# Kernel tuning notes

Measured on AMD Instinct MI355X. Metric: run time of the kernel, lower is better.

Reference implementation:

```python
import jax, jax.numpy as jnp
import numpy as np

ARITY = 4
DEPTH = 8  # leaves live at level DEPTH; levels 0..DEPTH, BFS layout
N_NODES = (ARITY ** (DEPTH + 1) - 1) // (ARITY - 1)  # 87381
V, E, H = 1024, 128, 128


def _offset(level):
    return (ARITY ** level - 1) // (ARITY - 1)


def _lstm_final(seq, w_ih, w_hh, b):
    # seq: [T, B, E_in] -> final hidden state [B, H] (torch LSTM cell, gate order i,f,g,o)
    B = seq.shape[1]
    Hh = w_hh.shape[1]
    xg = jnp.einsum('tbe,ge->tbg', seq, w_ih) + b  # precompute input projections [T,B,4H]

    def step(carry, g_t):
        h, c = carry
        g = g_t + h @ w_hh.T
        i, f, gg, o = jnp.split(g, 4, axis=-1)
        c = jax.nn.sigmoid(f) * c + jax.nn.sigmoid(i) * jnp.tanh(gg)
        h = jax.nn.sigmoid(o) * jnp.tanh(c)
        return (h, c), None

    init = (jnp.zeros((B, Hh), seq.dtype), jnp.zeros((B, Hh), seq.dtype))
    (h, _), _ = jax.lax.scan(step, init, xg)
    return h


def setup_inputs():
    key = jax.random.key(0)
    ks = jax.random.split(key, 12)
    s = 0.1
    labels = jax.random.randint(ks[0], (N_NODES,), 0, V)
    emb = jax.random.normal(ks[1], (V, E), jnp.float32) * s
    emb = emb.at[0].set(0.0)  # padding_idx=0
    mk = lambda k, shp: jax.random.normal(k, shp, jnp.float32) * s
    return {
        'labels': labels, 'emb': emb,
        'w_ih_f': mk(ks[2], (4 * H, E)), 'w_hh_f': mk(ks[3], (4 * H, H)),
        'b_ih_f': mk(ks[4], (4 * H,)), 'b_hh_f': mk(ks[5], (4 * H,)),
        'w_ih_b': mk(ks[6], (4 * H, E)), 'w_hh_b': mk(ks[7], (4 * H, H)),
        'b_ih_b': mk(ks[8], (4 * H,)), 'b_hh_b': mk(ks[9], (4 * H,)),
        'lin_w': mk(ks[10], (E, 2 * H)), 'lin_b': mk(ks[11], (E,)),
    }


def reference(labels, emb, w_ih_f, w_hh_f, b_ih_f, b_hh_f,
              w_ih_b, w_hh_b, b_ih_b, b_hh_b, lin_w, lin_b):
    # padding row is frozen at zero (padding_idx=0 semantics)
    emb = emb.at[0].set(0.0)
    node_emb = emb[labels]  # [N, E]
    bf = b_ih_f + b_hh_f
    bb = b_ih_b + b_hh_b
    enc = jnp.zeros((N_NODES, E), node_emb.dtype)
    # level-by-level dynamic batching: identical math to per-node recursion
    for level in range(DEPTH, -1, -1):
        start = _offset(level)
        count = ARITY ** level
        x = node_emb[start:start + count]  # [C, E]
        if level == DEPTH:
            seq = jnp.stack([x, x])  # leaves: [node, node] -> [2, C, E]
        else:
            cstart = _offset(level + 1)
            ch = enc[cstart:cstart + count * ARITY]
            ch = ch.reshape(count, ARITY, E).transpose(1, 0, 2)  # [K, C, E]
            seq = jnp.concatenate([x[None], ch, x[None]], axis=0)  # [K+2, C, E]
        h_f = _lstm_final(seq, w_ih_f, w_hh_f, bf)          # forward direction
        h_b = _lstm_final(seq[::-1], w_ih_b, w_hh_b, bb)    # reverse direction
        out = jnp.tanh(jnp.concatenate([h_f, h_b], axis=-1) @ lin_w.T + lin_b)
        enc = enc.at[start:start + count].set(out)
    return enc[0]  # root encoding, shape [E]
```

## Files before the change

### kernel.cpp

```cpp
#include <hip/hip_runtime.h>
#include <hip/hip_bf16.h>

typedef __attribute__((ext_vector_type(8))) short bf16x8;
typedef __attribute__((ext_vector_type(4))) float f32x4;

__device__ __forceinline__ ushort f2bf(float f) {
  union { float f; unsigned u; } v; v.f = f;
  unsigned u = v.u;
  return (ushort)((u + 0x7FFFu + ((u >> 16) & 1u)) >> 16);
}
__device__ __forceinline__ float bf2f(ushort u) {
  union { unsigned u; float f; } v; v.u = ((unsigned)u) << 16;
  return v.f;
}
__device__ __forceinline__ float fsig(float x) {
  return __builtin_amdgcn_rcpf(1.0f + __expf(-x));
}
__device__ __forceinline__ float ftnh(float x) {
  float e = __expf(2.0f * x);
  return 1.0f - 2.0f * __builtin_amdgcn_rcpf(e + 1.0f);
}
__device__ __forceinline__ f32x4 MF(bf16x8 a, bf16x8 b, f32x4 c) {
  return __builtin_amdgcn_mfma_f32_16x16x32_bf16(a, b, c, 0, 0, 0);
}

__global__ __launch_bounds__(256) void repack_all2(
    const float* __restrict__ wihf, const float* __restrict__ whhf,
    const float* __restrict__ wihb, const float* __restrict__ whhb,
    const float* __restrict__ emb, const float* __restrict__ linw,
    ushort* __restrict__ wall) {
  int i = blockIdx.x * 256 + threadIdx.x;
  if (i < 131072) {
    int e = i & 7, f = (i >> 3) & 15, lane = (i >> 7) & 63, w = (i >> 13) & 7,
        d = (i >> 16) & 1;
    int nt = f >> 2, kk = f & 3;
    int pcol = w * 64 + nt * 16 + (lane & 15);
    int g = (pcol >> 4) & 3, h = (pcol >> 6) * 16 + (pcol & 15);
    int k = kk * 32 + (lane >> 4) * 8 + e;
    const float* src = d ? whhb : whhf;
    wall[i] = f2bf(src[(g * 128 + h) * 128 + k]);
  } else if (i < 262144) {
    int r = i - 131072;
    int e = r & 7, lane = (r >> 3) & 63, kk = (r >> 9) & 3, j = (r >> 11) & 7,
        wq = (r >> 14) & 3, d = (r >> 16) & 1;
    int pcol = wq * 128 + j * 16 + (lane & 15);
    int g = (pcol >> 4) & 3, h = (pcol >> 6) * 16 + (pcol & 15);
    int k = kk * 32 + (lane >> 4) * 8 + e;
    const float* src = d ? wihb : wihf;
    wall[i] = f2bf(src[(g * 128 + h) * 128 + k]);
  } else if (i < 294912) {
    int r = i - 262144;
    int e = r & 7, lane = (r >> 3) & 63, kk = (r >> 9) & 7, w = (r >> 12) & 7;
    int col = w * 16 + (lane & 15);
    int k = kk * 32 + (lane >> 4) * 8 + e;
    wall[i] = f2bf(linw[col * 256 + k]);
  } else if (i < 425984) {
    int r = i - 294912;
    wall[i] = f2bf(emb[r]);
  }
}

__global__ __launch_bounds__(512) void vocab_all(
    const ushort* __restrict__ emb_bf, const ushort* __restrict__ wihrep,
    const ushort* __restrict__ whhrep, const ushort* __restrict__ linrep,
    const float* __restrict__ linb, const float* __restrict__ bihf,
    const float* __restrict__ bhhf, const float* __restrict__ bihb,
    const float* __restrict__ bhhb, ushort* __restrict__ gxv,
    ushort* __restrict__ gcv) {
  __shared__ __align__(16) ushort sT[2048];
  __shared__ __align__(16) ushort sGx[16384];
  __shared__ __align__(16) ushort sHf[2][2048];
  __shared__ __align__(16) ushort sH[2048];
  const int tid = threadIdx.x;
  const int w = tid >> 6, l = tid & 63, hlo = l & 15, lg = l >> 4;
  const int r0 = lg * 4, k0 = lg * 8;
  const int hcol = w * 16 + hlo;
  const int v0 = blockIdx.x * 16;

  {
    int row = tid >> 5, col0 = (tid & 31) * 4;
    *(ushort4*)(sT + row * 128 + (col0 ^ ((row & 7) << 3))) =
        *(const ushort4*)(emb_bf + (size_t)(v0 + row) * 128 + col0);
  }
  __syncthreads();
  const int dd = w >> 2, wq = w & 3;
  {
    const ushort* wp = wihrep + (size_t)(dd * 4 + wq) * 16384 + l * 8;
    bf16x8 wfv[32];
#pragma unroll
    for (int j = 0; j < 8; ++j)
#pragma unroll
      for (int kk = 0; kk < 4; ++kk)
        wfv[j * 4 + kk] = *(const bf16x8*)(wp + j * 2048 + kk * 512);
    bf16x8 a[4];
#pragma unroll
    for (int kk = 0; kk < 4; ++kk)
      a[kk] = *(const bf16x8*)(sT + hlo * 128 + ((kk * 32 + k0) ^ ((hlo & 7) << 3)));
    f32x4 acc[8];
#pragma unroll
    for (int j = 0; j < 8; ++j) { f32x4 z = {0.f, 0.f, 0.f, 0.f}; acc[j] = z; }
#pragma unroll
    for (int kk = 0; kk < 4; ++kk)
#pragma unroll
      for (int j = 0; j < 8; ++j) acc[j] = MF(a[kk], wfv[j * 4 + kk], acc[j]);
#pragma unroll
    for (int p = 0; p < 2; ++p)
#pragma unroll
      for (int rg = 0; rg < 4; ++rg) {
        int hid = (wq * 2 + p) * 16 + hlo;
        ushort4 q = {f2bf(acc[p * 4 + 0][rg]), f2bf(acc[p * 4 + 1][rg]),
                     f2bf(acc[p * 4 + 2][rg]), f2bf(acc[p * 4 + 3][rg])};
        *(ushort4*)(gxv + (size_t)(v0 + r0 + rg) * 1024 + dd * 512 + hid * 4) = q;
        *(ushort4*)(sGx + (r0 + rg) * 1024 + dd * 512 + hid * 4) = q;
      }
  }
  __syncthreads();

  for (int d = 0; d < 2; ++d) {
    bf16x8 whh[16];
    {
      const ushort* p = whhrep + d * 65536 + w * 8192 + l * 128;
#pragma unroll
      for (int f = 0; f < 16; ++f) whh[f] = *(const bf16x8*)(p + f * 8);
    }
    const float* bih = d ? bihb : bihf;
    const float* bhh = d ? bhhb : bhhf;
    float bs[4];
#pragma unroll
    for (int nt = 0; nt < 4; ++nt)
      bs[nt] = bih[nt * 128 + hcol] + bhh[nt * 128 + hcol];
    ushort4 xg[4];
#pragma unroll
    for (int rg = 0; rg < 4; ++rg)
      xg[rg] = *(const ushort4*)(sGx + (r0 + rg) * 1024 + d * 512 + hcol * 4);
    float c_st[4], hn[4];
#pragma unroll
    for (int rg = 0; rg < 4; ++rg) {
      float g0 = bf2f(xg[rg].x) + bs[0];
      float g2 = bf2f(xg[rg].z) + bs[2];
      float g3 = bf2f(xg[rg].w) + bs[3];
      float c = fsig(g0) * ftnh(g2);
      c_st[rg] = c;
      hn[rg] = fsig(g3) * ftnh(c);
    }
#pragma unroll
    for (int rg = 0; rg < 4; ++rg) {
      int rr = r0 + rg;
      sH[rr * 128 + (hcol ^ ((rr & 7) << 3))] = f2bf(hn[rg]);
    }
    __syncthreads();
    f32x4 a4[4];
#pragma unroll
    for (int rg = 0; rg < 4; ++rg)
#pragma unroll
      for (int nt = 0; nt < 4; ++nt)
        a4[nt][rg] = bf2f(((const ushort*)&xg[rg])[nt]) + bs[nt];
    bf16x8 ah[4];
#pragma unroll
    for (int kk = 0; kk < 4; ++kk)
      ah[kk] = *(const bf16x8*)(sH + hlo * 128 + ((kk * 32 + k0) ^ ((hlo & 7) << 3)));
#pragma unroll
    for (int kk = 0; kk < 4; ++kk)
#pragma unroll
      for (int nt = 0; nt < 4; ++nt) a4[nt] = MF(ah[kk], whh[nt * 4 + kk], a4[nt]);
#pragma unroll
    for (int rg = 0; rg < 4; ++rg) {
      float iv = fsig(a4[0][rg]);
      float fv = fsig(a4[1][rg]);
      float gv = ftnh(a4[2][rg]);
      float ov = fsig(a4[3][rg]);
      float c = fv * c_st[rg] + iv * gv;
      int rr = r0 + rg;
      sHf[d][rr * 128 + (hcol ^ ((rr & 7) << 3))] = f2bf(ov * ftnh(c));
    }
    __syncthreads();
  }

  {
    const float lb = linb[hcol];
    f32x4 hac = {lb, lb, lb, lb};
#pragma unroll
    for (int kk = 0; kk < 8; ++kk) {
      bf16x8 lfr = *(const bf16x8*)(linrep + w * 4096 + kk * 512 + l * 8);
      bf16x8 af = *(const bf16x8*)(&sHf[kk >> 2][0] + hlo * 128 +
                                   (((kk & 3) * 32 + k0) ^ ((hlo & 7) << 3)));
      hac = MF(af, lfr, hac);
    }
#pragma unroll
    for (int rg = 0; rg < 4; ++rg) {
      int rr = r0 + rg;
      sT[rr * 128 + (hcol ^ ((rr & 7) << 3))] = f2bf(ftnh(hac[rg]));
    }
    __syncthreads();
    const ushort* wp = wihrep + (size_t)(dd * 4 + wq) * 16384 + l * 8;
    bf16x8 a[4];
#pragma unroll
    for (int kk = 0; kk < 4; ++kk)
      a[kk] = *(const bf16x8*)(sT + hlo * 128 + ((kk * 32 + k0) ^ ((hlo & 7) << 3)));
    f32x4 acc[8];
#pragma unroll
    for (int j = 0; j < 8; ++j) { f32x4 z = {0.f, 0.f, 0.f, 0.f}; acc[j] = z; }
#pragma unroll
    for (int kk = 0; kk < 4; ++kk)
#pragma unroll
      for (int j = 0; j < 8; ++j) {
        bf16x8 wf = *(const bf16x8*)(wp + j * 2048 + kk * 512);
        acc[j] = MF(a[kk], wf, acc[j]);
      }
#pragma unroll
    for (int p = 0; p < 2; ++p)
#pragma unroll
      for (int rg = 0; rg < 4; ++rg) {
        int hid = (wq * 2 + p) * 16 + hlo;
        ushort4 q = {f2bf(acc[p * 4 + 0][rg]), f2bf(acc[p * 4 + 1][rg]),
                     f2bf(acc[p * 4 + 2][rg]), f2bf(acc[p * 4 + 3][rg])};
        *(ushort4*)(gcv + (size_t)(v0 + r0 + rg) * 1024 + dd * 512 + hid * 4) = q;
      }
  }
}

template <bool CLAB>
__global__ __launch_bounds__(512, 2) void scan_lvl2(
    const int* __restrict__ xlab, const int* __restrict__ clab,
    const ushort* __restrict__ gxv, const ushort* __restrict__ gsrc,
    const ushort* __restrict__ wihrep, const ushort* __restrict__ whhrep,
    const ushort* __restrict__ linrep, const float* __restrict__ linb,
    const float* __restrict__ bihf, const float* __restrict__ bhhf,
    const float* __restrict__ bihb, const float* __restrict__ bhhb,
    ushort* __restrict__ gdst) {
  __shared__ __align__(16) ushort sH[2][2048];
  __shared__ __align__(16) ushort sHF[2][2048];
  __shared__ __align__(16) ushort sT[2048];

  const int tid = threadIdx.x;
  const int w = tid >> 6, l = tid & 63, hlo = l & 15, lg = l >> 4;
  const int r0 = lg * 4, k0 = lg * 8;
  const int hcol = w * 16 + hlo;
  const int axswz = (hlo & 7) << 3;
  const int n0 = blockIdx.x * 16;

  for (int d = 0; d < 2; ++d) {
    bf16x8 whh[16];
    {
      const ushort* p = whhrep + d * 65536 + w * 8192 + l * 128;
#pragma unroll
      for (int f = 0; f < 16; ++f) whh[f] = *(const bf16x8*)(p + f * 8);
    }
    const float* bih = d ? bihb : bihf;
    const float* bhh = d ? bhhb : bhhf;
    float bs[4];
#pragma unroll
    for (int nt = 0; nt < 4; ++nt)
      bs[nt] = bih[nt * 128 + hcol] + bhh[nt * 128 + hcol];

    float c_st[4];
    {
      ushort4 xg[4];
#pragma unroll
      for (int rg = 0; rg < 4; ++rg) {
        int n = n0 + r0 + rg;
        xg[rg] = *(const ushort4*)(gxv + (size_t)xlab[n] * 1024 + d * 512 + hcol * 4);
      }
#pragma unroll
      for (int rg = 0; rg < 4; ++rg) {
        float g0 = bf2f(xg[rg].x) + bs[0];
        float g2 = bf2f(xg[rg].z) + bs[2];
        float g3 = bf2f(xg[rg].w) + bs[3];
        float c = fsig(g0) * ftnh(g2);
        c_st[rg] = c;
        float h = fsig(g3) * ftnh(c);
        int rr = r0 + rg;
        sH[0][rr * 128 + (hcol ^ ((rr & 7) << 3))] = f2bf(h);
      }
    }
    __syncthreads();

#pragma unroll
    for (int t = 1; t < 6; ++t) {
      ushort4 gv[4];
      if (t < 5) {
        const int ci = d ? (4 - t) : (t - 1);
#pragma unroll
        for (int rg = 0; rg < 4; ++rg) {
          int n = n0 + r0 + rg;
          size_t row = CLAB ? (size_t)clab[4 * n + ci] : (size_t)(4 * n + ci);
          gv[rg] = *(const ushort4*)(gsrc + row * 1024 + d * 512 + hcol * 4);
        }
      } else {
#pragma unroll
        for (int rg = 0; rg < 4; ++rg) {
          int n = n0 + r0 + rg;
          gv[rg] = *(const ushort4*)(gxv + (size_t)xlab[n] * 1024 + d * 512 + hcol * 4);
        }
      }
      f32x4 a4[4];
#pragma unroll
      for (int nt = 0; nt < 4; ++nt) {
        f32x4 z = {bs[nt], bs[nt], bs[nt], bs[nt]};
        a4[nt] = z;
      }
      bf16x8 ah[4];
#pragma unroll
      for (int kk = 0; kk < 4; ++kk)
        ah[kk] = *(const bf16x8*)(&sH[(t + 1) & 1][0] + hlo * 128 +
                                  ((kk * 32 + k0) ^ axswz));
#pragma unroll
      for (int kk = 0; kk < 4; ++kk)
#pragma unroll
        for (int nt = 0; nt < 4; ++nt) a4[nt] = MF(ah[kk], whh[nt * 4 + kk], a4[nt]);
#pragma unroll
      for (int rg = 0; rg < 4; ++rg) {
        a4[0][rg] += bf2f(gv[rg].x);
        a4[1][rg] += bf2f(gv[rg].y);
        a4[2][rg] += bf2f(gv[rg].z);
        a4[3][rg] += bf2f(gv[rg].w);
      }
      float hn[4];
#pragma unroll
      for (int rg = 0; rg < 4; ++rg) {
        float iv = fsig(a4[0][rg]);
        float fv = fsig(a4[1][rg]);
        float gg = ftnh(a4[2][rg]);
        float ov = fsig(a4[3][rg]);
        float c = fv * c_st[rg] + iv * gg;
        c_st[rg] = c;
        hn[rg] = ov * ftnh(c);
      }
      ushort* dstp = (t < 5) ? &sH[t & 1][0] : &sHF[d][0];
#pragma unroll
      for (int rg = 0; rg < 4; ++rg) {
        int rr = r0 + rg;
        dstp[rr * 128 + (hcol ^ ((rr & 7) << 3))] = f2bf(hn[rg]);
      }
      __syncthreads();
    }
  }

  const int dd = w >> 2, wq = w & 3;
  const float lb = linb[hcol];
  f32x4 hac = {lb, lb, lb, lb};
#pragma unroll
  for (int kk = 0; kk < 8; ++kk) {
    bf16x8 lfr = *(const bf16x8*)(linrep + w * 4096 + kk * 512 + l * 8);
    bf16x8 af = *(const bf16x8*)(&sHF[kk >> 2][0] + hlo * 128 +
                                 (((kk & 3) * 32 + k0) ^ axswz));
    hac = MF(af, lfr, hac);
  }
#pragma unroll
  for (int rg = 0; rg < 4; ++rg) {
    int rr = r0 + rg;
    sT[rr * 128 + (hcol ^ ((rr & 7) << 3))] = f2bf(ftnh(hac[rg]));
  }
  __syncthreads();
  bf16x8 a[4];
#pragma unroll
  for (int kk = 0; kk < 4; ++kk)
    a[kk] = *(const bf16x8*)(sT + hlo * 128 + ((kk * 32 + k0) ^ axswz));
#pragma unroll
  for (int half = 0; half < 2; ++half) {
    const ushort* wp =
        wihrep + (size_t)(dd * 4 + wq) * 16384 + (size_t)(half * 4) * 2048 + l * 8;
    f32x4 acc[4];
#pragma unroll
    for (int j = 0; j < 4; ++j) { f32x4 z = {0.f, 0.f, 0.f, 0.f}; acc[j] = z; }
#pragma unroll
    for (int kk = 0; kk < 4; ++kk)
#pragma unroll
      for (int j = 0; j < 4; ++j) {
        bf16x8 wf = *(const bf16x8*)(wp + j * 2048 + kk * 512);
        acc[j] = MF(a[kk], wf, acc[j]);
      }
    const int hid = (wq * 2 + half) * 16 + hlo;
#pragma unroll
    for (int rg = 0; rg < 4; ++rg) {
      int n = n0 + r0 + rg;
      ushort4 q = {f2bf(acc[0][rg]), f2bf(acc[1][rg]), f2bf(acc[2][rg]),
                   f2bf(acc[3][rg])};
      *(ushort4*)(gdst + (size_t)n * 1024 + dd * 512 + hid * 4) = q;
    }
  }
}

__global__ __launch_bounds__(512) void tail_lvls(
    const int* __restrict__ labels, const ushort* __restrict__ gxv,
    const ushort* __restrict__ gc3, const ushort* __restrict__ wihrep,
    const ushort* __restrict__ whhrep, const ushort* __restrict__ linrep,
    const float* __restrict__ linb, const float* __restrict__ bihf,
    const float* __restrict__ bhhf, const float* __restrict__ bihb,
    const float* __restrict__ bhhb, float* __restrict__ outp) {
  __shared__ __align__(16) ushort sH[2][2048];
  __shared__ __align__(16) ushort sHF[2][2048];
  __shared__ __align__(16) ushort sT[2048];
  __shared__ __align__(16) ushort sGc[16384];

  const int tid = threadIdx.x;
  const int w = tid >> 6, l = tid & 63, hlo = l & 15, lg = l >> 4;
  const int r0 = lg * 4, k0 = lg * 8;
  const int hcol = w * 16 + hlo;
  const int axswz = (hlo & 7) << 3;
  const int dd = w >> 2, wq = w & 3;

  bf16x8 lf[8];
#pragma unroll
  for (int kk = 0; kk < 8; ++kk)
    lf[kk] = *(const bf16x8*)(linrep + w * 4096 + kk * 512 + l * 8);
  const float lb = linb[hcol];
  const int cnts[3] = {16, 4, 1};
  const int xoffs[3] = {5, 1, 0};

  for (int p = 0; p < 3; ++p) {
    const int cnt = cnts[p];
    const int* xlab = labels + xoffs[p];
    const ushort* gsrc = (p == 0) ? gc3 : (const ushort*)sGc;
    int nnr[4];
#pragma unroll
    for (int rg = 0; rg < 4; ++rg) {
      int n = r0 + rg;
      nnr[rg] = (n < cnt) ? n : (cnt - 1);
    }

    for (int d = 0; d < 2; ++d) {
      bf16x8 whh[16];
      {
        const ushort* pw = whhrep + d * 65536 + w * 8192 + l * 128;
#pragma unroll
        for (int f = 0; f < 16; ++f) whh[f] = *(const bf16x8*)(pw + f * 8);
      }
      const float* bih = d ? bihb : bihf;
      const float* bhh = d ? bhhb : bhhf;
      float bs[4];
#pragma unroll
      for (int nt = 0; nt < 4; ++nt)
        bs[nt] = bih[nt * 128 + hcol] + bhh[nt * 128 + hcol];

      ushort4 xg[4];
#pragma unroll
      for (int rg = 0; rg < 4; ++rg)
        xg[rg] = *(const ushort4*)(gxv + (size_t)xlab[nnr[rg]] * 1024 +
                                   d * 512 + hcol * 4);
      float c_st[4];
#pragma unroll
      for (int t = 0; t < 6; ++t) {
        const bool isx = (t == 0) || (t == 5);
        f32x4 a4[4];
#pragma unroll
        for (int rg = 0; rg < 4; ++rg) {
          ushort4 u;
          if (isx) {
            u = xg[rg];
          } else {
            const int ci = d ? (4 - t) : (t - 1);
            int row = 4 * nnr[rg] + ci;
            u = *(const ushort4*)(gsrc + (size_t)row * 1024 + d * 512 + hcol * 4);
          }
#pragma unroll
          for (int nt = 0; nt < 4; ++nt)
            a4[nt][rg] = bf2f(((const ushort*)&u)[nt]) + bs[nt];
        }
        if (t > 0) {
          bf16x8 ah[4];
#pragma unroll
          for (int kk = 0; kk < 4; ++kk)
            ah[kk] = *(const bf16x8*)(&sH[(t + 1) & 1][0] + hlo * 128 +
                                      ((kk * 32 + k0) ^ axswz));
#pragma unroll
          for (int kk = 0; kk < 4; ++kk)
#pragma unroll
            for (int nt = 0; nt < 4; ++nt)
              a4[nt] = MF(ah[kk], whh[nt * 4 + kk], a4[nt]);
        }
        float hn[4];
#pragma unroll
        for (int rg = 0; rg < 4; ++rg) {
          float iv = fsig(a4[0][rg]);
          float fv = fsig(a4[1][rg]);
          float gv = ftnh(a4[2][rg]);
          float ov = fsig(a4[3][rg]);
          float c = (t == 0) ? (iv * gv) : (fv * c_st[rg] + iv * gv);
          c_st[rg] = c;
          hn[rg] = ov * ftnh(c);
        }
        ushort* dstp = (t < 5) ? &sH[t & 1][0] : &sHF[d][0];
#pragma unroll
        for (int rg = 0; rg < 4; ++rg) {
          int rr = r0 + rg;
          dstp[rr * 128 + (hcol ^ ((rr & 7) << 3))] = f2bf(hn[rg]);
        }
        __syncthreads();
      }
    }

    f32x4 hac = {lb, lb, lb, lb};
#pragma unroll
    for (int kk = 0; kk < 8; ++kk) {
      bf16x8 af = *(const bf16x8*)(&sHF[kk >> 2][0] + hlo * 128 +
                                   (((kk & 3) * 32 + k0) ^ axswz));
      hac = MF(af, lf[kk], hac);
    }
    if (p == 2) {
      if (lg == 0) outp[hcol] = ftnh(hac[0]);
      return;
    }
    __syncthreads();
#pragma unroll
    for (int rg = 0; rg < 4; ++rg) {
      int rr = r0 + rg;
      sT[rr * 128 + (hcol ^ ((rr & 7) << 3))] = f2bf(ftnh(hac[rg]));
    }
    __syncthreads();
    bf16x8 a[4];
#pragma unroll
    for (int kk = 0; kk < 4; ++kk)
      a[kk] = *(const bf16x8*)(sT + hlo * 128 + ((kk * 32 + k0) ^ axswz));
    f32x4 acc[8];
#pragma unroll
    for (int j = 0; j < 8; ++j) { f32x4 z = {0.f, 0.f, 0.f, 0.f}; acc[j] = z; }
    const ushort* wp = wihrep + (size_t)(dd * 4 + wq) * 16384 + l * 8;
#pragma unroll
    for (int kk = 0; kk < 4; ++kk)
#pragma unroll
      for (int j = 0; j < 8; ++j) {
        bf16x8 wf = *(const bf16x8*)(wp + j * 2048 + kk * 512);
        acc[j] = MF(a[kk], wf, acc[j]);
      }
#pragma unroll
    for (int pp = 0; pp < 2; ++pp)
#pragma unroll
      for (int rg = 0; rg < 4; ++rg) {
        int n = r0 + rg;
        if (n < cnt) {
          int hid = (wq * 2 + pp) * 16 + hlo;
          ushort4 q = {f2bf(acc[pp * 4 + 0][rg]), f2bf(acc[pp * 4 + 1][rg]),
                       f2bf(acc[pp * 4 + 2][rg]), f2bf(acc[pp * 4 + 3][rg])};
          *(ushort4*)(sGc + (size_t)n * 1024 + dd * 512 + hid * 4) = q;
        }
      }
    __syncthreads();
  }
}

extern "C" void kernel_launch(void* const* d_in, const int* in_sizes, int n_in,
                              void* d_out, int out_size, void* d_ws, size_t ws_size,
                              hipStream_t stream) {
  const int* labels = (const int*)d_in[0];
  const float* emb = (const float*)d_in[1];
  const float* w_ih_f = (const float*)d_in[2];
  const float* w_hh_f = (const float*)d_in[3];
  const float* b_ih_f = (const float*)d_in[4];
  const float* b_hh_f = (const float*)d_in[5];
  const float* w_ih_b = (const float*)d_in[6];
  const float* w_hh_b = (const float*)d_in[7];
  const float* b_ih_b = (const float*)d_in[8];
  const float* b_hh_b = (const float*)d_in[9];
  const float* lin_w = (const float*)d_in[10];
  const float* lin_b = (const float*)d_in[11];
  float* out = (float*)d_out;

  ushort* gxv = (ushort*)d_ws;
  ushort* gcA = gxv + 1048576;
  ushort* gcB = gcA + 16777216;
  ushort* gcv = gcB;
  ushort* wall = gcB + 4194304;
  ushort* whhrep = wall;
  ushort* wihrep = wall + 131072;
  ushort* linrep = wall + 262144;
  ushort* emb_bf = wall + 294912;

  repack_all2<<<1664, 256, 0, stream>>>(w_ih_f, w_hh_f, w_ih_b, w_hh_b, emb,
                                        lin_w, wall);
  vocab_all<<<64, 512, 0, stream>>>(emb_bf, wihrep, whhrep, linrep, lin_b,
                                    b_ih_f, b_hh_f, b_ih_b, b_hh_b, gxv, gcv);
  scan_lvl2<true><<<1024, 512, 0, stream>>>(
      labels + 5461, labels + 21845, gxv, gcv, wihrep, whhrep, linrep, lin_b,
      b_ih_f, b_hh_f, b_ih_b, b_hh_b, gcA);
  scan_lvl2<false><<<256, 512, 0, stream>>>(
      labels + 1365, nullptr, gxv, gcA, wihrep, whhrep, linrep, lin_b, b_ih_f,
      b_hh_f, b_ih_b, b_hh_b, gcB);
  scan_lvl2<false><<<64, 512, 0, stream>>>(
      labels + 341, nullptr, gxv, gcB, wihrep, whhrep, linrep, lin_b, b_ih_f,
      b_hh_f, b_ih_b, b_hh_b, gcA);
  scan_lvl2<false><<<16, 512, 0, stream>>>(
      labels + 85, nullptr, gxv, gcA, wihrep, whhrep, linrep, lin_b, b_ih_f,
      b_hh_f, b_ih_b, b_hh_b, gcB);
  scan_lvl2<false><<<4, 512, 0, stream>>>(
      labels + 21, nullptr, gxv, gcB, wihrep, whhrep, linrep, lin_b, b_ih_f,
      b_hh_f, b_ih_b, b_hh_b, gcA);
  tail_lvls<<<1, 512, 0, stream>>>(labels, gxv, gcA, wihrep, whhrep, linrep,
                                   lin_b, b_ih_f, b_hh_f, b_ih_b, b_hh_b, out);
}
```

Before: 308.1 us.

## Process multiple 16-node tiles per block in level scan to amortize weight loads

The level-scan kernel is templated on MT so one block handles MT 16-node tiles. The recurrent weight fragments held in registers and the linear weight fragments are then loaded once per block and reused across tiles. The largest level launches 256 blocks of 4 tiles instead of 1024 single-tile blocks. Node and child labels are staged in shared memory once per block. Launch bounds drop to one block per CU, which trades occupancy and latency hiding for fewer weight reloads and more independent MFMA work per synchronization.

```diff
diff --git a/kernel.cpp b/kernel.cpp
--- a/kernel.cpp
+++ b/kernel.cpp
@@ -219,8 +219,8 @@
   }
 }
 
-template <bool CLAB>
-__global__ __launch_bounds__(512, 2) void scan_lvl2(
+template <int MT, bool CLAB>
+__global__ __launch_bounds__(512, 1) void scan_lvl3(
     const int* __restrict__ xlab, const int* __restrict__ clab,
     const ushort* __restrict__ gxv, const ushort* __restrict__ gsrc,
     const ushort* __restrict__ wihrep, const ushort* __restrict__ whhrep,
@@ -228,16 +228,23 @@
     const float* __restrict__ bihf, const float* __restrict__ bhhf,
     const float* __restrict__ bihb, const float* __restrict__ bhhb,
     ushort* __restrict__ gdst) {
-  __shared__ __align__(16) ushort sH[2][2048];
-  __shared__ __align__(16) ushort sHF[2][2048];
+  __shared__ __align__(16) ushort sH[2][MT * 2048];
+  __shared__ __align__(16) ushort sHF[2][MT * 2048];
   __shared__ __align__(16) ushort sT[2048];
+  __shared__ int sLabX[MT * 16];
+  __shared__ int sLabC[CLAB ? MT * 64 : 1];
 
   const int tid = threadIdx.x;
   const int w = tid >> 6, l = tid & 63, hlo = l & 15, lg = l >> 4;
   const int r0 = lg * 4, k0 = lg * 8;
   const int hcol = w * 16 + hlo;
   const int axswz = (hlo & 7) << 3;
-  const int n0 = blockIdx.x * 16;
+  const int n0 = blockIdx.x * (MT * 16);
+
+  for (int i = tid; i < MT * 16; i += 512) sLabX[i] = xlab[n0 + i];
+  if (CLAB)
+    for (int i = tid; i < MT * 64; i += 512) sLabC[i] = clab[4 * n0 + i];
+  __syncthreads();
 
   for (int d = 0; d < 2; ++d) {
     bf16x8 whh[16];
@@ -253,13 +260,15 @@
     for (int nt = 0; nt < 4; ++nt)
       bs[nt] = bih[nt * 128 + hcol] + bhh[nt * 128 + hcol];
 
-    float c_st[4];
-    {
+    float c_st[MT][4];
+#pragma unroll
+    for (int mt = 0; mt < MT; ++mt) {
       ushort4 xg[4];
 #pragma unroll
       for (int rg = 0; rg < 4; ++rg) {
-        int n = n0 + r0 + rg;
-        xg[rg] = *(const ushort4*)(gxv + (size_t)xlab[n] * 1024 + d * 512 + hcol * 4);
+        int ln = mt * 16 + r0 + rg;
+        xg[rg] = *(const ushort4*)(gxv + (size_t)sLabX[ln] * 1024 + d * 512 +
+                                   hcol * 4);
       }
 #pragma unroll
       for (int rg = 0; rg < 4; ++rg) {
@@ -267,70 +276,81 @@
         float g2 = bf2f(xg[rg].z) + bs[2];
         float g3 = bf2f(xg[rg].w) + bs[3];
         float c = fsig(g0) * ftnh(g2);
-        c_st[rg] = c;
+        c_st[mt][rg] = c;
         float h = fsig(g3) * ftnh(c);
         int rr = r0 + rg;
-        sH[0][rr * 128 + (hcol ^ ((rr & 7) << 3))] = f2bf(h);
+        sH[0][mt * 2048 + rr * 128 + (hcol ^ ((rr & 7) << 3))] = f2bf(h);
       }
     }
     __syncthreads();
 
 #pragma unroll
     for (int t = 1; t < 6; ++t) {
-      ushort4 gv[4];
+      ushort4 gv[MT][4];
       if (t < 5) {
         const int ci = d ? (4 - t) : (t - 1);
 #pragma unroll
+        for (int mt = 0; mt < MT; ++mt)
+#pragma unroll
+          for (int rg = 0; rg < 4; ++rg) {
+            int ln = mt * 16 + r0 + rg;
+            size_t row =
+                CLAB ? (size_t)sLabC[ln * 4 + ci] : (size_t)(4 * (n0 + ln) + ci);
+            gv[mt][rg] = *(const ushort4*)(gsrc + row * 1024 + d * 512 + hcol * 4);
+          }
+      } else {
+#pragma unroll
+        for (int mt = 0; mt < MT; ++mt)
+#pragma unroll
+          for (int rg = 0; rg < 4; ++rg) {
+            int ln = mt * 16 + r0 + rg;
+            gv[mt][rg] = *(const ushort4*)(gxv + (size_t)sLabX[ln] * 1024 +
+                                           d * 512 + hcol * 4);
+          }
+      }
+#pragma unroll
+      for (int mt = 0; mt < MT; ++mt) {
+        f32x4 a4[4];
+#pragma unroll
+        for (int nt = 0; nt < 4; ++nt) {
+          f32x4 z = {bs[nt], bs[nt], bs[nt], bs[nt]};
+          a4[nt] = z;
+        }
+        bf16x8 ah[4];
+#pragma unroll
+        for (int kk = 0; kk < 4; ++kk)
+          ah[kk] = *(const bf16x8*)(&sH[(t + 1) & 1][mt * 2048] + hlo * 128 +
+                                    ((kk * 32 + k0) ^ axswz));
+#pragma unroll
+        for (int kk = 0; kk < 4; ++kk)
+#pragma unroll
+          for (int nt = 0; nt < 4; ++nt)
+            a4[nt] = MF(ah[kk], whh[nt * 4 + kk], a4[nt]);
+#pragma unroll
         for (int rg = 0; rg < 4; ++rg) {
-          int n = n0 + r0 + rg;
-          size_t row = CLAB ? (size_t)clab[4 * n + ci] : (size_t)(4 * n + ci);
-          gv[rg] = *(const ushort4*)(gsrc + row * 1024 + d * 512 + hcol * 4);
-        }
-      } else {
+          a4[0][rg] += bf2f(gv[mt][rg].x);
+          a4[1][rg] += bf2f(gv[mt][rg].y);
+          a4[2][rg] += bf2f(gv[mt][rg].z);
+          a4[3][rg] += bf2f(gv[mt][rg].w);
+        }
+        float hn[4];
 #pragma unroll
         for (int rg = 0; rg < 4; ++rg) {
-          int n = n0 + r0 + rg;
-          gv[rg] = *(const ushort4*)(gxv + (size_t)xlab[n] * 1024 + d * 512 + hcol * 4);
-        }
-      }
-      f32x4 a4[4];
-#pragma unroll
-      for (int nt = 0; nt < 4; ++nt) {
-        f32x4 z = {bs[nt], bs[nt], bs[nt], bs[nt]};
-        a4[nt] = z;
-      }
-      bf16x8 ah[4];
-#pragma unroll
-      for (int kk = 0; kk < 4; ++kk)
-        ah[kk] = *(const bf16x8*)(&sH[(t + 1) & 1][0] + hlo * 128 +
-                                  ((kk * 32 + k0) ^ axswz));
-#pragma unroll
-      for (int kk = 0; kk < 4; ++kk)
-#pragma unroll
-        for (int nt = 0; nt < 4; ++nt) a4[nt] = MF(ah[kk], whh[nt * 4 + kk], a4[nt]);
-#pragma unroll
-      for (int rg = 0; rg < 4; ++rg) {
-        a4[0][rg] += bf2f(gv[rg].x);
-        a4[1][rg] += bf2f(gv[rg].y);
-        a4[2][rg] += bf2f(gv[rg].z);
-        a4[3][rg] += bf2f(gv[rg].w);
-      }
-      float hn[4];
-#pragma unroll
-      for (int rg = 0; rg < 4; ++rg) {
-        float iv = fsig(a4[0][rg]);
-        float fv = fsig(a4[1][rg]);
-        float gg = ftnh(a4[2][rg]);
-        float ov = fsig(a4[3][rg]);
-        float c = fv * c_st[rg] + iv * gg;
-        c_st[rg] = c;
-        hn[rg] = ov * ftnh(c);
-      }
-      ushort* dstp = (t < 5) ? &sH[t & 1][0] : &sHF[d][0];
-#pragma unroll
-      for (int rg = 0; rg < 4; ++rg) {
-        int rr = r0 + rg;
-        dstp[rr * 128 + (hcol ^ ((rr & 7) << 3))] = f2bf(hn[rg]);
+          float iv = fsig(a4[0][rg]);
+          float fv = fsig(a4[1][rg]);
+          float gg = ftnh(a4[2][rg]);
+          float ov = fsig(a4[3][rg]);
+          float c = fv * c_st[mt][rg] + iv * gg;
+          c_st[mt][rg] = c;
+          hn[rg] = ov * ftnh(c);
+        }
+        ushort* dstp =
+            (t < 5) ? &sH[t & 1][mt * 2048] : &sHF[d][mt * 2048];
+#pragma unroll
+        for (int rg = 0; rg < 4; ++rg) {
+          int rr = r0 + rg;
+          dstp[rr * 128 + (hcol ^ ((rr & 7) << 3))] = f2bf(hn[rg]);
+        }
       }
       __syncthreads();
     }
@@ -338,45 +358,52 @@
 
   const int dd = w >> 2, wq = w & 3;
   const float lb = linb[hcol];
-  f32x4 hac = {lb, lb, lb, lb};
-#pragma unroll
-  for (int kk = 0; kk < 8; ++kk) {
-    bf16x8 lfr = *(const bf16x8*)(linrep + w * 4096 + kk * 512 + l * 8);
-    bf16x8 af = *(const bf16x8*)(&sHF[kk >> 2][0] + hlo * 128 +
-                                 (((kk & 3) * 32 + k0) ^ axswz));
-    hac = MF(af, lfr, hac);
-  }
-#pragma unroll
-  for (int rg = 0; rg < 4; ++rg) {
-    int rr = r0 + rg;
-    sT[rr * 128 + (hcol ^ ((rr & 7) << 3))] = f2bf(ftnh(hac[rg]));
-  }
-  __syncthreads();
-  bf16x8 a[4];
-#pragma unroll
-  for (int kk = 0; kk < 4; ++kk)
-    a[kk] = *(const bf16x8*)(sT + hlo * 128 + ((kk * 32 + k0) ^ axswz));
-#pragma unroll
-  for (int half = 0; half < 2; ++half) {
-    const ushort* wp =
-        wihrep + (size_t)(dd * 4 + wq) * 16384 + (size_t)(half * 4) * 2048 + l * 8;
-    f32x4 acc[4];
-#pragma unroll
-    for (int j = 0; j < 4; ++j) { f32x4 z = {0.f, 0.f, 0.f, 0.f}; acc[j] = z; }
-#pragma unroll
-    for (int kk = 0; kk < 4; ++kk)
-#pragma unroll
-      for (int j = 0; j < 4; ++j) {
-        bf16x8 wf = *(const bf16x8*)(wp + j * 2048 + kk * 512);
-        acc[j] = MF(a[kk], wf, acc[j]);
-      }
-    const int hid = (wq * 2 + half) * 16 + hlo;
+  bf16x8 lf[8];
+#pragma unroll
+  for (int kk = 0; kk < 8; ++kk)
+    lf[kk] = *(const bf16x8*)(linrep + w * 4096 + kk * 512 + l * 8);
+#pragma unroll
+  for (int mt = 0; mt < MT; ++mt) {
+    f32x4 hac = {lb, lb, lb, lb};
+#pragma unroll
+    for (int kk = 0; kk < 8; ++kk) {
+      bf16x8 af = *(const bf16x8*)(&sHF[kk >> 2][mt * 2048] + hlo * 128 +
+                                   (((kk & 3) * 32 + k0) ^ axswz));
+      hac = MF(af, lf[kk], hac);
+    }
+    __syncthreads();
 #pragma unroll
     for (int rg = 0; rg < 4; ++rg) {
-      int n = n0 + r0 + rg;
-      ushort4 q = {f2bf(acc[0][rg]), f2bf(acc[1][rg]), f2bf(acc[2][rg]),
-                   f2bf(acc[3][rg])};
-      *(ushort4*)(gdst + (size_t)n * 1024 + dd * 512 + hid * 4) = q;
+      int rr = r0 + rg;
+      sT[rr * 128 + (hcol ^ ((rr & 7) << 3))] = f2bf(ftnh(hac[rg]));
+    }
+    __syncthreads();
+    bf16x8 a[4];
+#pragma unroll
+    for (int kk = 0; kk < 4; ++kk)
+      a[kk] = *(const bf16x8*)(sT + hlo * 128 + ((kk * 32 + k0) ^ axswz));
+#pragma unroll
+    for (int half = 0; half < 2; ++half) {
+      const ushort* wp = wihrep + (size_t)(dd * 4 + wq) * 16384 +
+                         (size_t)(half * 4) * 2048 + l * 8;
+      f32x4 acc[4];
+#pragma unroll
+      for (int j = 0; j < 4; ++j) { f32x4 z = {0.f, 0.f, 0.f, 0.f}; acc[j] = z; }
+#pragma unroll
+      for (int kk = 0; kk < 4; ++kk)
+#pragma unroll
+        for (int j = 0; j < 4; ++j) {
+          bf16x8 wf = *(const bf16x8*)(wp + j * 2048 + kk * 512);
+          acc[j] = MF(a[kk], wf, acc[j]);
+        }
+      const int hid = (wq * 2 + half) * 16 + hlo;
+#pragma unroll
+      for (int rg = 0; rg < 4; ++rg) {
+        int n = n0 + mt * 16 + r0 + rg;
+        ushort4 q = {f2bf(acc[0][rg]), f2bf(acc[1][rg]), f2bf(acc[2][rg]),
+                     f2bf(acc[3][rg])};
+        *(ushort4*)(gdst + (size_t)n * 1024 + dd * 512 + hid * 4) = q;
+      }
     }
   }
 }
@@ -570,19 +597,19 @@
                                         lin_w, wall);
   vocab_all<<<64, 512, 0, stream>>>(emb_bf, wihrep, whhrep, linrep, lin_b,
                                     b_ih_f, b_hh_f, b_ih_b, b_hh_b, gxv, gcv);
-  scan_lvl2<true><<<1024, 512, 0, stream>>>(
+  scan_lvl3<4, true><<<256, 512, 0, stream>>>(
       labels + 5461, labels + 21845, gxv, gcv, wihrep, whhrep, linrep, lin_b,
       b_ih_f, b_hh_f, b_ih_b, b_hh_b, gcA);
-  scan_lvl2<false><<<256, 512, 0, stream>>>(
+  scan_lvl3<1, false><<<256, 512, 0, stream>>>(
       labels + 1365, nullptr, gxv, gcA, wihrep, whhrep, linrep, lin_b, b_ih_f,
       b_hh_f, b_ih_b, b_hh_b, gcB);
-  scan_lvl2<false><<<64, 512, 0, stream>>>(
+  scan_lvl3<1, false><<<64, 512, 0, stream>>>(
       labels + 341, nullptr, gxv, gcB, wihrep, whhrep, linrep, lin_b, b_ih_f,
       b_hh_f, b_ih_b, b_hh_b, gcA);
-  scan_lvl2<false><<<16, 512, 0, stream>>>(
+  scan_lvl3<1, false><<<16, 512, 0, stream>>>(
       labels + 85, nullptr, gxv, gcA, wihrep, whhrep, linrep, lin_b, b_ih_f,
       b_hh_f, b_ih_b, b_hh_b, gcB);
-  scan_lvl2<false><<<4, 512, 0, stream>>>(
+  scan_lvl3<1, false><<<4, 512, 0, stream>>>(
       labels + 21, nullptr, gxv, gcB, wihrep, whhrep, linrep, lin_b, b_ih_f,
       b_hh_f, b_ih_b, b_hh_b, gcA);
   tail_lvls<<<1, 512, 0, stream>>>(labels, gxv, gcA, wihrep, whhrep, linrep,
```

Result: faster. 272.5 us (-11.6%).

## Process 64 nodes per block at level 7 and prefetch child gates

Applied to the files above, without the earlier changes.

Adds a scan7 kernel for the largest internal level that handles 64 nodes per block (four 16-row tiles). It reuses the per-direction W_hh register fragments and the linear/W_ih weights across four tiles and caches labels in shared memory, which reduces redundant weight loads and block count. The smaller-level kernel now software-prefetches the next timestep's gate rows one step ahead and precomputes row offsets. In exchange, scan7 uses more shared memory and registers, at one block per CU.

```diff
diff --git a/kernel.cpp b/kernel.cpp
--- a/kernel.cpp
+++ b/kernel.cpp
@@ -219,8 +219,192 @@
   }
 }
 
+__global__ __launch_bounds__(512, 1) void scan7(
+    const int* __restrict__ xlab, const int* __restrict__ clab,
+    const ushort* __restrict__ gxv, const ushort* __restrict__ gsrc,
+    const ushort* __restrict__ wihrep, const ushort* __restrict__ whhrep,
+    const ushort* __restrict__ linrep, const float* __restrict__ linb,
+    const float* __restrict__ bihf, const float* __restrict__ bhhf,
+    const float* __restrict__ bihb, const float* __restrict__ bhhb,
+    ushort* __restrict__ gdst) {
+  __shared__ __align__(16) ushort sH[2][8192];
+  __shared__ __align__(16) ushort sHF[2][8192];
+  __shared__ __align__(16) ushort sT4[4][2048];
+  __shared__ int sLabX[64];
+  __shared__ int sLabC[256];
+
+  const int tid = threadIdx.x;
+  const int w = tid >> 6, l = tid & 63, hlo = l & 15, lg = l >> 4;
+  const int r0 = lg * 4, k0 = lg * 8;
+  const int hcol = w * 16 + hlo;
+  const int axswz = (hlo & 7) << 3;
+  const int n0 = blockIdx.x * 64;
+  const int gofs = hcol * 4;
+
+  for (int i = tid; i < 64; i += 512) sLabX[i] = xlab[n0 + i] << 10;
+  for (int i = tid; i < 256; i += 512) sLabC[i] = clab[4 * n0 + i] << 10;
+  __syncthreads();
+
+  for (int d = 0; d < 2; ++d) {
+    bf16x8 whh[16];
+    {
+      const ushort* p = whhrep + d * 65536 + w * 8192 + l * 128;
+#pragma unroll
+      for (int f = 0; f < 16; ++f) whh[f] = *(const bf16x8*)(p + f * 8);
+    }
+    const float* bih = d ? bihb : bihf;
+    const float* bhh = d ? bhhb : bhhf;
+    float bs[4];
+#pragma unroll
+    for (int nt = 0; nt < 4; ++nt)
+      bs[nt] = bih[nt * 128 + hcol] + bhh[nt * 128 + hcol];
+    const int dof = d * 512 + gofs;
+
+    float c_st[4][4];
+#pragma unroll
+    for (int mt = 0; mt < 4; ++mt) {
+      ushort4 xg[4];
+#pragma unroll
+      for (int rg = 0; rg < 4; ++rg)
+        xg[rg] = *(const ushort4*)(gxv + (size_t)(sLabX[mt * 16 + r0 + rg] + dof));
+#pragma unroll
+      for (int rg = 0; rg < 4; ++rg) {
+        float g0 = bf2f(xg[rg].x) + bs[0];
+        float g2 = bf2f(xg[rg].z) + bs[2];
+        float g3 = bf2f(xg[rg].w) + bs[3];
+        float c = fsig(g0) * ftnh(g2);
+        c_st[mt][rg] = c;
+        float h = fsig(g3) * ftnh(c);
+        int rr = r0 + rg;
+        sH[0][mt * 2048 + rr * 128 + (hcol ^ ((rr & 7) << 3))] = f2bf(h);
+      }
+    }
+    __syncthreads();
+
+#pragma unroll
+    for (int t = 1; t < 6; ++t) {
+      ushort4 gv[4][4];
+      if (t < 5) {
+        const int ci = d ? (4 - t) : (t - 1);
+#pragma unroll
+        for (int mt = 0; mt < 4; ++mt)
+#pragma unroll
+          for (int rg = 0; rg < 4; ++rg)
+            gv[mt][rg] = *(const ushort4*)(gsrc +
+                (size_t)(sLabC[(mt * 16 + r0 + rg) * 4 + ci] + dof));
+      } else {
+#pragma unroll
+        for (int mt = 0; mt < 4; ++mt)
+#pragma unroll
+          for (int rg = 0; rg < 4; ++rg)
+            gv[mt][rg] = *(const ushort4*)(gxv +
+                (size_t)(sLabX[mt * 16 + r0 + rg] + dof));
+      }
+#pragma unroll
+      for (int mt = 0; mt < 4; ++mt) {
+        f32x4 a4[4];
+#pragma unroll
+        for (int nt = 0; nt < 4; ++nt) {
+          f32x4 z = {bs[nt], bs[nt], bs[nt], bs[nt]};
+          a4[nt] = z;
+        }
+        bf16x8 ah[4];
+#pragma unroll
+        for (int kk = 0; kk < 4; ++kk)
+          ah[kk] = *(const bf16x8*)(&sH[(t + 1) & 1][mt * 2048] + hlo * 128 +
+                                    ((kk * 32 + k0) ^ axswz));
+#pragma unroll
+        for (int kk = 0; kk < 4; ++kk)
+#pragma unroll
+          for (int nt = 0; nt < 4; ++nt)
+            a4[nt] = MF(ah[kk], whh[nt * 4 + kk], a4[nt]);
+#pragma unroll
+        for (int rg = 0; rg < 4; ++rg) {
+          a4[0][rg] += bf2f(gv[mt][rg].x);
+          a4[1][rg] += bf2f(gv[mt][rg].y);
+          a4[2][rg] += bf2f(gv[mt][rg].z);
+          a4[3][rg] += bf2f(gv[mt][rg].w);
+        }
+        float hn[4];
+#pragma unroll
+        for (int rg = 0; rg < 4; ++rg) {
+          float iv = fsig(a4[0][rg]);
+          float fv = fsig(a4[1][rg]);
+          float gg = ftnh(a4[2][rg]);
+          float ov = fsig(a4[3][rg]);
+          float c = fv * c_st[mt][rg] + iv * gg;
+          c_st[mt][rg] = c;
+          hn[rg] = ov * ftnh(c);
+        }
+        ushort* dstp = (t < 5) ? &sH[t & 1][mt * 2048] : &sHF[d][mt * 2048];
+#pragma unroll
+        for (int rg = 0; rg < 4; ++rg) {
+          int rr = r0 + rg;
+          dstp[rr * 128 + (hcol ^ ((rr & 7) << 3))] = f2bf(hn[rg]);
+        }
+      }
+      __syncthreads();
+    }
+  }
+
+  const int dd = w >> 2, wq = w & 3;
+  const float lb = linb[hcol];
+  {
+    bf16x8 lf[8];
+#pragma unroll
+    for (int kk = 0; kk < 8; ++kk)
+      lf[kk] = *(const bf16x8*)(linrep + w * 4096 + kk * 512 + l * 8);
+#pragma unroll
+    for (int mt = 0; mt < 4; ++mt) {
+      f32x4 hac = {lb, lb, lb, lb};
+#pragma unroll
+      for (int kk = 0; kk < 8; ++kk) {
+        bf16x8 af = *(const bf16x8*)(&sHF[kk >> 2][mt * 2048] + hlo * 128 +
+                                     (((kk & 3) * 32 + k0) ^ axswz));
+        hac = MF(af, lf[kk], hac);
+      }
+#pragma unroll
+      for (int rg = 0; rg < 4; ++rg) {
+        int rr = r0 + rg;
+        sT4[mt][rr * 128 + (hcol ^ ((rr & 7) << 3))] = f2bf(ftnh(hac[rg]));
+      }
+    }
+  }
+  __syncthreads();
+#pragma unroll
+  for (int mt = 0; mt < 4; ++mt) {
+    bf16x8 a[4];
+#pragma unroll
+    for (int kk = 0; kk < 4; ++kk)
+      a[kk] = *(const bf16x8*)(&sT4[mt][0] + hlo * 128 + ((kk * 32 + k0) ^ axswz));
+#pragma unroll
+    for (int half = 0; half < 2; ++half) {
+      const ushort* wp = wihrep + (size_t)(dd * 4 + wq) * 16384 +
+                         (size_t)(half * 4) * 2048 + l * 8;
+      f32x4 acc[4];
+#pragma unroll
+      for (int j = 0; j < 4; ++j) { f32x4 z = {0.f, 0.f, 0.f, 0.f}; acc[j] = z; }
+#pragma unroll
+      for (int kk = 0; kk < 4; ++kk)
+#pragma unroll
+        for (int j = 0; j < 4; ++j) {
+          bf16x8 wf = *(const bf16x8*)(wp + j * 2048 + kk * 512);
+          acc[j] = MF(a[kk], wf, acc[j]);
+        }
+      const int hid = (wq * 2 + half) * 16 + hlo;
+#pragma unroll
+      for (int rg = 0; rg < 4; ++rg) {
+        int n = n0 + mt * 16 + r0 + rg;
+        ushort4 q = {f2bf(acc[0][rg]), f2bf(acc[1][rg]), f2bf(acc[2][rg]),
+                     f2bf(acc[3][rg])};
+        *(ushort4*)(gdst + (size_t)n * 1024 + dd * 512 + hid * 4) = q;
+      }
+    }
+  }
+}
+
 template <bool CLAB>
-__global__ __launch_bounds__(512, 2) void scan_lvl2(
+__global__ __launch_bounds__(512, 2) void scan_small(
     const int* __restrict__ xlab, const int* __restrict__ clab,
     const ushort* __restrict__ gxv, const ushort* __restrict__ gsrc,
     const ushort* __restrict__ wihrep, const ushort* __restrict__ whhrep,
@@ -238,6 +422,15 @@
   const int hcol = w * 16 + hlo;
   const int axswz = (hlo & 7) << 3;
   const int n0 = blockIdx.x * 16;
+  const int gofs = hcol * 4;
+
+  int xrow[4], crow[4];
+#pragma unroll
+  for (int rg = 0; rg < 4; ++rg) {
+    int n = n0 + r0 + rg;
+    xrow[rg] = xlab[n] << 10;
+    crow[rg] = CLAB ? 0 : ((4 * n) << 10);
+  }
 
   for (int d = 0; d < 2; ++d) {
     bf16x8 whh[16];
@@ -252,15 +445,15 @@
 #pragma unroll
     for (int nt = 0; nt < 4; ++nt)
       bs[nt] = bih[nt * 128 + hcol] + bhh[nt * 128 + hcol];
+    const int dof = d * 512 + gofs;
 
     float c_st[4];
+    ushort4 gv[4];
     {
       ushort4 xg[4];
 #pragma unroll
-      for (int rg = 0; rg < 4; ++rg) {
-        int n = n0 + r0 + rg;
-        xg[rg] = *(const ushort4*)(gxv + (size_t)xlab[n] * 1024 + d * 512 + hcol * 4);
-      }
+      for (int rg = 0; rg < 4; ++rg)
+        xg[rg] = *(const ushort4*)(gxv + (size_t)(xrow[rg] + dof));
 #pragma unroll
       for (int rg = 0; rg < 4; ++rg) {
         float g0 = bf2f(xg[rg].x) + bs[0];
@@ -273,25 +466,32 @@
         sH[0][rr * 128 + (hcol ^ ((rr & 7) << 3))] = f2bf(h);
       }
     }
+    {
+      const int ci = d ? 3 : 0;
+#pragma unroll
+      for (int rg = 0; rg < 4; ++rg) {
+        int row = CLAB ? (clab[4 * (n0 + r0 + rg) + ci] << 10)
+                       : (crow[rg] + (ci << 10));
+        gv[rg] = *(const ushort4*)(gsrc + (size_t)(row + dof));
+      }
+    }
     __syncthreads();
 
 #pragma unroll
     for (int t = 1; t < 6; ++t) {
-      ushort4 gv[4];
-      if (t < 5) {
-        const int ci = d ? (4 - t) : (t - 1);
+      ushort4 gvn[4];
+      if (t < 4) {
+        const int ci = d ? (3 - t) : t;
 #pragma unroll
         for (int rg = 0; rg < 4; ++rg) {
-          int n = n0 + r0 + rg;
-          size_t row = CLAB ? (size_t)clab[4 * n + ci] : (size_t)(4 * n + ci);
-          gv[rg] = *(const ushort4*)(gsrc + row * 1024 + d * 512 + hcol * 4);
-        }
-      } else {
-#pragma unroll
-        for (int rg = 0; rg < 4; ++rg) {
-          int n = n0 + r0 + rg;
-          gv[rg] = *(const ushort4*)(gxv + (size_t)xlab[n] * 1024 + d * 512 + hcol * 4);
-        }
+          int row = CLAB ? (clab[4 * (n0 + r0 + rg) + ci] << 10)
+                         : (crow[rg] + (ci << 10));
+          gvn[rg] = *(const ushort4*)(gsrc + (size_t)(row + dof));
+        }
+      } else if (t == 4) {
+#pragma unroll
+        for (int rg = 0; rg < 4; ++rg)
+          gvn[rg] = *(const ushort4*)(gxv + (size_t)(xrow[rg] + dof));
       }
       f32x4 a4[4];
 #pragma unroll
@@ -331,6 +531,10 @@
       for (int rg = 0; rg < 4; ++rg) {
         int rr = r0 + rg;
         dstp[rr * 128 + (hcol ^ ((rr & 7) << 3))] = f2bf(hn[rg]);
+      }
+      if (t < 5) {
+#pragma unroll
+        for (int rg = 0; rg < 4; ++rg) gv[rg] = gvn[rg];
       }
       __syncthreads();
     }
@@ -570,19 +774,19 @@
                                         lin_w, wall);
   vocab_all<<<64, 512, 0, stream>>>(emb_bf, wihrep, whhrep, linrep, lin_b,
                                     b_ih_f, b_hh_f, b_ih_b, b_hh_b, gxv, gcv);
-  scan_lvl2<true><<<1024, 512, 0, stream>>>(
-      labels + 5461, labels + 21845, gxv, gcv, wihrep, whhrep, linrep, lin_b,
-      b_ih_f, b_hh_f, b_ih_b, b_hh_b, gcA);
-  scan_lvl2<false><<<256, 512, 0, stream>>>(
+  scan7<<<256, 512, 0, stream>>>(labels + 5461, labels + 21845, gxv, gcv,
+                                 wihrep, whhrep, linrep, lin_b, b_ih_f, b_hh_f,
+                                 b_ih_b, b_hh_b, gcA);
+  scan_small<false><<<256, 512, 0, stream>>>(
       labels + 1365, nullptr, gxv, gcA, wihrep, whhrep, linrep, lin_b, b_ih_f,
       b_hh_f, b_ih_b, b_hh_b, gcB);
-  scan_lvl2<false><<<64, 512, 0, stream>>>(
+  scan_small<false><<<64, 512, 0, stream>>>(
       labels + 341, nullptr, gxv, gcB, wihrep, whhrep, linrep, lin_b, b_ih_f,
       b_hh_f, b_ih_b, b_hh_b, gcA);
-  scan_lvl2<false><<<16, 512, 0, stream>>>(
+  scan_small<false><<<16, 512, 0, stream>>>(
       labels + 85, nullptr, gxv, gcA, wihrep, whhrep, linrep, lin_b, b_ih_f,
       b_hh_f, b_ih_b, b_hh_b, gcB);
-  scan_lvl2<false><<<4, 512, 0, stream>>>(
+  scan_small<false><<<4, 512, 0, stream>>>(
       labels + 21, nullptr, gxv, gcB, wihrep, whhrep, linrep, lin_b, b_ih_f,
       b_hh_f, b_ih_b, b_hh_b, gcA);
   tail_lvls<<<1, 512, 0, stream>>>(labels, gxv, gcA, wihrep, whhrep, linrep,
```

Measured after the change: 266.5 us. -13.5%, faster.
